# Optimization experiments

Measured on AMD Instinct MI355X. Metric: run time of the kernel, lower is better.

## Reference

```python
import jax, jax.numpy as jnp
import numpy as np

B, N, NEV, E, D, L = 4, 20000, 100000, 400000, 64, 3

def setup_inputs() -> dict:
    key = jax.random.key(0)
    ks = jax.random.split(key, 12)
    x = jax.random.normal(ks[0], (B, N, 3), dtype=jnp.float32)
    # channel 0 is the susceptible boolean mask (0/1)
    mask0 = (jax.random.uniform(ks[1], (B, N)) < 0.3).astype(jnp.float32)
    x = x.at[..., 0].set(mask0)
    dag_edge_index = jax.random.randint(ks[2], (2, E), 0, NEV, dtype=jnp.int64)
    event_to_node = jax.random.randint(ks[3], (NEV,), 0, N, dtype=jnp.int64)
    event_src_node = jax.random.randint(ks[4], (NEV,), 0, N, dtype=jnp.int64)
    s = 1.0 / np.sqrt(D)
    Wp = jax.random.normal(ks[5], (6, D), dtype=jnp.float32) * (1.0 / np.sqrt(6))
    bp = jnp.zeros((D,), dtype=jnp.float32)
    Ws = jax.random.normal(ks[6], (L, D, D), dtype=jnp.float32) * s
    Wa = jax.random.normal(ks[7], (L, D, D), dtype=jnp.float32) * s
    ba = jnp.zeros((L, D), dtype=jnp.float32)
    Wo = jax.random.normal(ks[8], (D,), dtype=jnp.float32) * s
    bo = jnp.zeros((), dtype=jnp.float32)
    return {"x": x, "Wp": Wp, "bp": bp, "Ws": Ws, "Wa": Wa, "ba": ba,
            "Wo": Wo, "bo": bo, "dag_edge_index": dag_edge_index,
            "event_to_node": event_to_node, "event_src_node": event_src_node}

def reference(x, Wp, bp, Ws, Wa, ba, Wo, bo, dag_edge_index, event_to_node, event_src_node):
    n_events = event_src_node.shape[0]
    # event features: [B, n_events, 6] -> project -> ReLU
    ev_feat = jnp.concatenate([x[:, event_src_node, :], x[:, event_to_node, :]], axis=-1)
    h = jax.nn.relu(ev_feat @ Wp + bp)  # [B, n_events, D]
    # reversed DAG edges: src = dag[1], dst = dag[0]
    src_e, dst_e = dag_edge_index[1], dag_edge_index[0]
    deg = jnp.zeros((n_events,), h.dtype).at[dst_e].add(1.0)
    deg = jnp.maximum(deg, 1.0)[None, :, None]
    for l in range(Ws.shape[0]):
        agg = jnp.zeros_like(h).at[:, dst_e].add(h[:, src_e])  # scatter-add mean agg
        h = jax.nn.relu(h @ Ws[l] + (agg / deg) @ Wa[l] + ba[l])
    # aggregate events back to nodes (mean)
    node_emb = jnp.zeros((x.shape[0], x.shape[1], h.shape[-1]), h.dtype).at[:, event_to_node].add(h)
    count = jnp.zeros((x.shape[1],), h.dtype).at[event_to_node].add(1.0)
    node_emb = node_emb / jnp.maximum(count, 1.0)[None, :, None]
    scores = node_emb @ Wo + bo  # [B, N]
    susceptible = x[..., 0] > 0
    scores = jnp.where(susceptible, -jnp.inf, scores)
    return jax.nn.log_softmax(scores, axis=-1)
```

## Files before the change

### kernel.cpp

```cpp
#include <hip/hip_runtime.h>
#include <hip/hip_bf16.h>
#include <math.h>

constexpr int B   = 4;
constexpr int N   = 20000;
constexpr int NEV = 100000;
constexpr int E   = 400000;
constexpr int D   = 64;
constexpr int L   = 3;
constexpr int CAP = 32;
constexpr int CHUNK = 625;

typedef short  short8 __attribute__((ext_vector_type(8)));
typedef float  f32x4  __attribute__((ext_vector_type(4)));
typedef float  f32x2  __attribute__((ext_vector_type(2)));


__device__ inline unsigned short f2bu(float f) {
  union { __hip_bfloat16 b; unsigned short s; } u;
  u.b = __float2bfloat16(f);
  return u.s;
}
__device__ inline unsigned packbf(float lo, float hi) {
  return ((unsigned)f2bu(hi) << 16) | (unsigned)f2bu(lo);
}
__device__ inline void cvt16(float* a, uint4 v) {
  unsigned vv[4] = {v.x, v.y, v.z, v.w};
#pragma unroll
  for (int i = 0; i < 4; ++i) {
    f32x2 lo = __builtin_amdgcn_cvt_pk_f32_fp8((int)vv[i], false);
    f32x2 hi = __builtin_amdgcn_cvt_pk_f32_fp8((int)vv[i], true);
    a[4 * i + 0] = lo[0]; a[4 * i + 1] = lo[1];
    a[4 * i + 2] = hi[0]; a[4 * i + 3] = hi[1];
  }
}
__device__ inline void add16(float* a, uint4 v) {
  unsigned vv[4] = {v.x, v.y, v.z, v.w};
#pragma unroll
  for (int i = 0; i < 4; ++i) {
    f32x2 lo = __builtin_amdgcn_cvt_pk_f32_fp8((int)vv[i], false);
    f32x2 hi = __builtin_amdgcn_cvt_pk_f32_fp8((int)vv[i], true);
    a[4 * i + 0] += lo[0]; a[4 * i + 1] += lo[1];
    a[4 * i + 2] += hi[0]; a[4 * i + 3] += hi[1];
  }
}
__device__ inline short8 pack8(const float* f) {
  union { unsigned u[4]; short8 s; } r;
#pragma unroll
  for (int i = 0; i < 4; ++i) r.u[i] = packbf(f[2 * i], f[2 * i + 1]);
  return r.s;
}


__global__ void k_zero(float4* __restrict__ p, int n4) {
  int i = blockIdx.x * blockDim.x + threadIdx.x;
  if (i < n4) p[i] = make_float4(0.f, 0.f, 0.f, 0.f);
}

__global__ void k_prep(const int* __restrict__ dag,
                       int* __restrict__ cnt,
                       int* __restrict__ csrc,
                       const int* __restrict__ e2n,
                       int* __restrict__ ncount,
                       const float* __restrict__ Ws,
                       const float* __restrict__ Wa,
                       unsigned short* __restrict__ Wt) {
  int bid = blockIdx.x;
  if (bid < 1563) {
    int i = bid * 256 + threadIdx.x;
    if (i < E) {
      int dst = dag[i];
      int src = dag[E + i];
      int pos = atomicAdd(&cnt[dst], 1);
      if (pos < CAP) csrc[dst * CAP + pos] = src;
    }
  } else if (bid < 1954) {
    int i = (bid - 1563) * 256 + threadIdx.x;
    if (i < NEV) atomicAdd(&ncount[e2n[i]], 1);
  } else {
    int i = (bid - 1954) * 256 + threadIdx.x;
    int l  = i >> 13;
    int r  = i & 8191;
    int n  = r >> 7;
    int s2 = r & 127;
    int hf = s2 >> 6, s = s2 & 63;
    int b  = ((s >> 3) & 3) * 16 + (s >> 5) * 8 + (s & 7);
    int c  = (b & 3) * 16 + (b >> 2);
    float v = hf ? Wa[l * 4096 + c * 64 + n]
                 : Ws[l * 4096 + c * 64 + n];
    Wt[l * 8192 + n * 128 + s2] = f2bu(v);
  }
}

__global__ __launch_bounds__(256) void k_proj(const float* __restrict__ x,
                                              const float* __restrict__ Wp,
                                              const float* __restrict__ bp,
                                              const int* __restrict__ esrc,
                                              const int* __restrict__ e2n,
                                              unsigned* __restrict__ h,
                                              float* __restrict__ nscore) {
  int gid = blockIdx.x * blockDim.x + threadIdx.x;
  if (gid < B * N) nscore[gid] = 0.f;
  const int lane = threadIdx.x & 63;
  const int e    = gid >> 6;
  int sn = esrc[e], tn = e2n[e];
  float xval = 0.f;
  if (lane < 24) {
    int bl = lane / 6, rem = lane % 6;
    int node = (rem < 3) ? sn : tn;
    xval = x[(size_t)(bl * N + node) * 3 + (rem < 3 ? rem : rem - 3)];
  }
  const int b = lane >> 4, p = lane & 15;
  float xv[6];
#pragma unroll
  for (int k = 0; k < 6; ++k) xv[k] = __shfl(xval, b * 6 + k, 64);
  float a[4];
#pragma unroll
  for (int t = 0; t < 4; ++t) {
    int d = p + 16 * t;
    float acc = bp[d];
#pragma unroll
    for (int k = 0; k < 6; ++k) acc += xv[k] * Wp[k * 64 + d];
    a[t] = fmaxf(acc, 0.f);
  }
  int w = __builtin_amdgcn_cvt_pk_fp8_f32(a[0], a[1], 0, false);
  w     = __builtin_amdgcn_cvt_pk_fp8_f32(a[2], a[3], w, true);
  h[e * 64 + lane] = (unsigned)w;
}

template <bool LAST>
__global__ __launch_bounds__(256, 4) void k_layer(
    const unsigned short* __restrict__ Wt,
    const float* __restrict__ ba,
    const float* __restrict__ Wo,
    const int* __restrict__ e2n,
    const int* __restrict__ cnt,
    const int* __restrict__ csrc,
    const unsigned char* __restrict__ h_in,
    unsigned char* __restrict__ h_out,
    float* __restrict__ nscore) {
  const int tid  = threadIdx.x;
  const int wv   = tid >> 6, lane = tid & 63;
  const int e0   = blockIdx.x * 16;
  const int r0   = e0 * 4;
  const int m    = lane & 15, q = lane >> 4;
  const int el   = m >> 2;
  const int bb   = m & 3;
  const int e_loc = wv * 4 + el;

  int vidx = csrc[(size_t)(e0 + wv * 4 + q) * CAP + m];

  uint4 vd = *(const uint4*)(h_in + (size_t)(r0 + wv * 16 + m) * 64 + q * 16);

  int c    = cnt[e0 + e_loc];
  int cc   = min(c, CAP);
  int cc16 = min(cc, 16);
  float a[16];
#pragma unroll
  for (int i = 0; i < 16; ++i) a[i] = 0.f;
  const unsigned char* gb = h_in + bb * 64 + q * 16;
  for (int p = 0; p < cc16; p += 4) {
    uint4 v[4];
#pragma unroll
    for (int t = 0; t < 4; ++t) {
      v[t] = make_uint4(0u, 0u, 0u, 0u);
      int j = p + t;
      int s = __shfl(vidx, (el << 4) | (j & 15), 64);
      if (j < cc16) v[t] = *(const uint4*)(gb + (size_t)s * 256);
    }
#pragma unroll
    for (int t = 0; t < 4; ++t) add16(a, v[t]);
  }
  for (int j = 16; j < cc; ++j) {
    int s = csrc[(size_t)(e0 + e_loc) * CAP + j];
    add16(a, *(const uint4*)(gb + (size_t)s * 256));
  }
  {
    float inv = 1.f / fmaxf((float)c, 1.f);
#pragma unroll
    for (int i = 0; i < 16; ++i) a[i] *= inv;
  }
  short8 ag0 = pack8(a), ag1 = pack8(a + 8);

  short8 ad0, ad1;
  {
    float fd[16];
    cvt16(fd, vd);
    ad0 = pack8(fd); ad1 = pack8(fd + 8);
  }

  f32x4 acc[4];
#pragma unroll
  for (int t = 0; t < 4; ++t) {
    float bv = ba[t * 16 + m];
    acc[t] = (f32x4){bv, bv, bv, bv};
  }
  const unsigned short* wb = Wt + m * 128 + q * 8;
#pragma unroll
  for (int t = 0; t < 4; ++t) {
    acc[t] = __builtin_amdgcn_mfma_f32_16x16x32_bf16(
        ad0, *(const short8*)(wb + t * 2048 + 0),  acc[t], 0, 0, 0);
    acc[t] = __builtin_amdgcn_mfma_f32_16x16x32_bf16(
        ad1, *(const short8*)(wb + t * 2048 + 32), acc[t], 0, 0, 0);
    acc[t] = __builtin_amdgcn_mfma_f32_16x16x32_bf16(
        ag0, *(const short8*)(wb + t * 2048 + 64), acc[t], 0, 0, 0);
    acc[t] = __builtin_amdgcn_mfma_f32_16x16x32_bf16(
        ag1, *(const short8*)(wb + t * 2048 + 96), acc[t], 0, 0, 0);
  }

  if constexpr (!LAST) {
#pragma unroll
    for (int r = 0; r < 4; ++r) {
      int w = __builtin_amdgcn_cvt_pk_fp8_f32(fmaxf(acc[0][r], 0.f),
                                              fmaxf(acc[1][r], 0.f), 0, false);
      w     = __builtin_amdgcn_cvt_pk_fp8_f32(fmaxf(acc[2][r], 0.f),
                                              fmaxf(acc[3][r], 0.f), w, true);
      int grow = r0 + wv * 16 + q * 4 + r;
      ((unsigned*)h_out)[grow * 16 + m] = (unsigned)w;
    }
  } else {
    float w0 = Wo[m], w1 = Wo[16 + m], w2 = Wo[32 + m], w3 = Wo[48 + m];
#pragma unroll
    for (int r = 0; r < 4; ++r) {
      float v = fmaxf(acc[0][r], 0.f) * w0 + fmaxf(acc[1][r], 0.f) * w1
              + fmaxf(acc[2][r], 0.f) * w2 + fmaxf(acc[3][r], 0.f) * w3;
      v += __shfl_xor(v, 1, 64);
      v += __shfl_xor(v, 2, 64);
      v += __shfl_xor(v, 4, 64);
      v += __shfl_xor(v, 8, 64);
      if (m == 0) {
        int grow = r0 + wv * 16 + q * 4 + r;
        int e = grow >> 2, b = grow & 3;
        atomicAdd(&nscore[b * N + e2n[e]], v);
      }
    }
  }
}

__device__ inline float ls_score(const float* nscore, const int* ncount,
                                 const float* x, float bov, int b, int n) {
  return (x[(size_t)(b * N + n) * 3] > 0.f)
             ? -INFINITY
             : nscore[b * N + n] / fmaxf((float)ncount[n], 1.f) + bov;
}

__global__ __launch_bounds__(256) void k_ls1(const float* __restrict__ nscore,
                                             const int* __restrict__ ncount,
                                             const float* __restrict__ x,
                                             const float* __restrict__ bo,
                                             float* __restrict__ pmax,
                                             float* __restrict__ psum,
                                             float* __restrict__ sc) {
  const int b = blockIdx.x >> 5, ch = blockIdx.x & 31;
  const int n0 = ch * CHUNK;
  const int tid = threadIdx.x;
  const float bov = bo[0];
  float s0 = -INFINITY, s1 = -INFINITY, s2 = -INFINITY;
  if (tid < CHUNK) {
    s0 = ls_score(nscore, ncount, x, bov, b, n0 + tid);
    sc[b * N + n0 + tid] = s0;
  }
  if (tid + 256 < CHUNK) {
    s1 = ls_score(nscore, ncount, x, bov, b, n0 + tid + 256);
    sc[b * N + n0 + tid + 256] = s1;
  }
  if (tid + 512 < CHUNK) {
    s2 = ls_score(nscore, ncount, x, bov, b, n0 + tid + 512);
    sc[b * N + n0 + tid + 512] = s2;
  }
  float m = fmaxf(fmaxf(s0, s1), s2);
  __shared__ float red[4];
#pragma unroll
  for (int o = 32; o; o >>= 1) m = fmaxf(m, __shfl_xor(m, o, 64));
  if ((tid & 63) == 0) red[tid >> 6] = m;
  __syncthreads();
  float pm = fmaxf(fmaxf(red[0], red[1]), fmaxf(red[2], red[3]));
  float pm2 = (pm == -INFINITY) ? 0.f : pm;
  float e = expf(s0 - pm2) + expf(s1 - pm2) + expf(s2 - pm2);
#pragma unroll
  for (int o = 32; o; o >>= 1) e += __shfl_xor(e, o, 64);
  __syncthreads();
  if ((tid & 63) == 0) red[tid >> 6] = e;
  __syncthreads();
  if (tid == 0) {
    pmax[blockIdx.x] = pm;
    psum[blockIdx.x] = red[0] + red[1] + red[2] + red[3];
  }
}

__global__ __launch_bounds__(256) void k_ls3(const float* __restrict__ pmax,
                                             const float* __restrict__ psum,
                                             const float* __restrict__ sc,
                                             float* __restrict__ out) {
  const int b = blockIdx.x >> 5, ch = blockIdx.x & 31;
  const int n0 = ch * CHUNK;
  const int tid = threadIdx.x;
  __shared__ float sgm, slse;
  if (tid < 64) {
    float pm = (tid < 32) ? pmax[b * 32 + tid] : -INFINITY;
    float ps = (tid < 32) ? psum[b * 32 + tid] : 0.f;
    float gm = pm;
#pragma unroll
    for (int o = 32; o; o >>= 1) gm = fmaxf(gm, __shfl_xor(gm, o, 64));
    float gm2 = (gm == -INFINITY) ? 0.f : gm;
    float c = (pm == -INFINITY) ? 0.f : ps * expf(pm - gm2);
#pragma unroll
    for (int o = 32; o; o >>= 1) c += __shfl_xor(c, o, 64);
    if (tid == 0) { sgm = gm; slse = logf(c); }
  }
  __syncthreads();
  const float gm = sgm, lse = slse;
  for (int i = tid; i < CHUNK; i += 256) {
    int n = n0 + i;
    out[b * N + n] = fmaxf(sc[b * N + n] - gm - lse, -3.0e38f);
  }
}

extern "C" void kernel_launch(void* const* d_in, const int* in_sizes, int n_in,
                              void* d_out, int out_size, void* d_ws, size_t ws_size,
                              hipStream_t stream) {
  const float* x   = (const float*)d_in[0];
  const float* Wp  = (const float*)d_in[1];
  const float* bp  = (const float*)d_in[2];
  const float* Ws  = (const float*)d_in[3];
  const float* Wa  = (const float*)d_in[4];
  const float* ba  = (const float*)d_in[5];
  const float* Wo  = (const float*)d_in[6];
  const float* bo  = (const float*)d_in[7];
  const int*   dag = (const int*)d_in[8];
  const int*   e2n = (const int*)d_in[9];
  const int*   esr = (const int*)d_in[10];

  int*   ws     = (int*)d_ws;
  int*   cnt    = ws;
  int*   ncount = ws + 100000;
  float* nscore = (float*)(ws + 120000);
  float* pmax   = (float*)(ws + 200000);
  float* psum   = (float*)(ws + 200128);
  int*   csrc   = ws + 200704;
  unsigned short* Wt = (unsigned short*)(ws + 3400704);
  unsigned char* h0 = (unsigned char*)(ws + 3406912);
  unsigned char* h1 = h0 + (size_t)B * NEV * D;
  float* sc     = (float*)(h1 + (size_t)B * NEV * D);
  float* out    = (float*)d_out;

  k_zero<<<(30000 + 255) / 256, 256, 0, stream>>>((float4*)ws, 30000);
  k_prep<<<2050, 256, 0, stream>>>(dag, cnt, csrc, e2n, ncount, Ws, Wa, Wt);
  k_proj<<<(B * NEV * 16) / 256, 256, 0, stream>>>(x, Wp, bp, esr, e2n,
                                                   (unsigned*)h0, nscore);

  k_layer<false><<<NEV / 16, 256, 0, stream>>>(Wt,         ba,       Wo, e2n,
                                               cnt, csrc, h0, h1, nscore);
  k_layer<false><<<NEV / 16, 256, 0, stream>>>(Wt + 8192,  ba + D,   Wo, e2n,
                                               cnt, csrc, h1, h0, nscore);
  k_layer<true><<<NEV / 16, 256, 0, stream>>>(Wt + 16384,  ba + 2*D, Wo, e2n,
                                              cnt, csrc, h0, h1, nscore);

  k_ls1<<<B * 32, 256, 0, stream>>>(nscore, ncount, x, bo, pmax, psum, sc);
  k_ls3<<<B * 32, 256, 0, stream>>>(pmax, psum, sc, out);
}
```

Baseline: 354.5 us.

## Process two event tiles per wave with sentinel-padded neighbor lists for gather ILP

Each layer block now handles 32 events instead of 16, with each wave computing two independent 16-row tiles (A and B). This interleaves their gathers and MFMAs for more memory-level parallelism and reuses the loaded weight fragments across both tiles. The CSR neighbor table is pre-filled with a sentinel index pointing at an extra zeroed row in each h buffer. This lets the first four neighbors be loaded unconditionally with vector int4 index loads instead of cross-lane shuffles and bounds checks. In exchange it adds a fill kernel, more registers per thread and half as many blocks, which may lower occupancy.

```diff
diff --git a/kernel.cpp b/kernel.cpp
--- a/kernel.cpp
+++ b/kernel.cpp
@@ -10,6 +10,7 @@
 constexpr int L   = 3;
 constexpr int CAP = 32;
 constexpr int CHUNK = 625;
+constexpr size_t HBYTES = (size_t)B * NEV * D + 256;
 
 typedef short  short8 __attribute__((ext_vector_type(8)));
 typedef float  f32x4  __attribute__((ext_vector_type(4)));
@@ -50,11 +51,29 @@
   for (int i = 0; i < 4; ++i) r.u[i] = packbf(f[2 * i], f[2 * i + 1]);
   return r.s;
 }
+__device__ __forceinline__ void round4(const unsigned char* gb,
+                                       const int* cr, int p, float* a) {
+  int4 idx = *(const int4*)(cr + p);
+  uint4 v0 = *(const uint4*)(gb + (size_t)idx.x * 256);
+  uint4 v1 = *(const uint4*)(gb + (size_t)idx.y * 256);
+  uint4 v2 = *(const uint4*)(gb + (size_t)idx.z * 256);
+  uint4 v3 = *(const uint4*)(gb + (size_t)idx.w * 256);
+  add16(a, v0); add16(a, v1); add16(a, v2); add16(a, v3);
+}
 
 
 __global__ void k_zero(float4* __restrict__ p, int n4) {
   int i = blockIdx.x * blockDim.x + threadIdx.x;
   if (i < n4) p[i] = make_float4(0.f, 0.f, 0.f, 0.f);
+}
+
+__global__ void k_fill(int4* __restrict__ csrc4,
+                       uint4* __restrict__ h0z, uint4* __restrict__ h1z) {
+  int i = blockIdx.x * blockDim.x + threadIdx.x;
+  if (i < NEV * CAP / 4) csrc4[i] = make_int4(NEV, NEV, NEV, NEV);
+  int z = i - NEV * CAP / 4;
+  if (z >= 0 && z < 16) h0z[z] = make_uint4(0u, 0u, 0u, 0u);
+  if (z >= 16 && z < 32) h1z[z - 16] = make_uint4(0u, 0u, 0u, 0u);
 }
 
 __global__ void k_prep(const int* __restrict__ dag,
@@ -141,97 +160,119 @@
     float* __restrict__ nscore) {
   const int tid  = threadIdx.x;
   const int wv   = tid >> 6, lane = tid & 63;
-  const int e0   = blockIdx.x * 16;
+  const int e0   = blockIdx.x * 32;
   const int r0   = e0 * 4;
   const int m    = lane & 15, q = lane >> 4;
   const int el   = m >> 2;
   const int bb   = m & 3;
-  const int e_loc = wv * 4 + el;
-
-  int vidx = csrc[(size_t)(e0 + wv * 4 + q) * CAP + m];
-
-  uint4 vd = *(const uint4*)(h_in + (size_t)(r0 + wv * 16 + m) * 64 + q * 16);
-
-  int c    = cnt[e0 + e_loc];
-  int cc   = min(c, CAP);
-  int cc16 = min(cc, 16);
-  float a[16];
-#pragma unroll
-  for (int i = 0; i < 16; ++i) a[i] = 0.f;
+  const int eA   = e0 + wv * 4 + el;
+  const int eB   = e0 + 16 + wv * 4 + el;
+
+  const int* crA = csrc + (size_t)eA * CAP;
+  const int* crB = csrc + (size_t)eB * CAP;
+  int4 iA = *(const int4*)crA;
+  int4 iB = *(const int4*)crB;
+  uint4 vdA = *(const uint4*)(h_in + (size_t)(r0 + wv * 16 + m) * 64 + q * 16);
+  uint4 vdB = *(const uint4*)(h_in + (size_t)(r0 + 64 + wv * 16 + m) * 64 + q * 16);
+  int cA = cnt[eA];
+  int cB = cnt[eB];
+
   const unsigned char* gb = h_in + bb * 64 + q * 16;
-  for (int p = 0; p < cc16; p += 4) {
-    uint4 v[4];
-#pragma unroll
-    for (int t = 0; t < 4; ++t) {
-      v[t] = make_uint4(0u, 0u, 0u, 0u);
-      int j = p + t;
-      int s = __shfl(vidx, (el << 4) | (j & 15), 64);
-      if (j < cc16) v[t] = *(const uint4*)(gb + (size_t)s * 256);
-    }
-#pragma unroll
-    for (int t = 0; t < 4; ++t) add16(a, v[t]);
-  }
-  for (int j = 16; j < cc; ++j) {
-    int s = csrc[(size_t)(e0 + e_loc) * CAP + j];
-    add16(a, *(const uint4*)(gb + (size_t)s * 256));
-  }
+  float aA[16], aB[16];
+#pragma unroll
+  for (int i = 0; i < 16; ++i) { aA[i] = 0.f; aB[i] = 0.f; }
   {
-    float inv = 1.f / fmaxf((float)c, 1.f);
-#pragma unroll
-    for (int i = 0; i < 16; ++i) a[i] *= inv;
-  }
-  short8 ag0 = pack8(a), ag1 = pack8(a + 8);
-
-  short8 ad0, ad1;
+    uint4 vA0 = *(const uint4*)(gb + (size_t)iA.x * 256);
+    uint4 vA1 = *(const uint4*)(gb + (size_t)iA.y * 256);
+    uint4 vA2 = *(const uint4*)(gb + (size_t)iA.z * 256);
+    uint4 vA3 = *(const uint4*)(gb + (size_t)iA.w * 256);
+    uint4 vB0 = *(const uint4*)(gb + (size_t)iB.x * 256);
+    uint4 vB1 = *(const uint4*)(gb + (size_t)iB.y * 256);
+    uint4 vB2 = *(const uint4*)(gb + (size_t)iB.z * 256);
+    uint4 vB3 = *(const uint4*)(gb + (size_t)iB.w * 256);
+    add16(aA, vA0); add16(aA, vA1); add16(aA, vA2); add16(aA, vA3);
+    add16(aB, vB0); add16(aB, vB1); add16(aB, vB2); add16(aB, vB3);
+  }
+  int ccA = min(cA, CAP), ccA16 = min(ccA, 16);
+  int ccB = min(cB, CAP), ccB16 = min(ccB, 16);
+  for (int p = 4; p < ccA16; p += 4) round4(gb, crA, p, aA);
+  for (int p = 4; p < ccB16; p += 4) round4(gb, crB, p, aB);
+  for (int j = 16; j < ccA; ++j)
+    add16(aA, *(const uint4*)(gb + (size_t)crA[j] * 256));
+  for (int j = 16; j < ccB; ++j)
+    add16(aB, *(const uint4*)(gb + (size_t)crB[j] * 256));
   {
-    float fd[16];
-    cvt16(fd, vd);
-    ad0 = pack8(fd); ad1 = pack8(fd + 8);
-  }
-
-  f32x4 acc[4];
+    float invA = 1.f / fmaxf((float)cA, 1.f);
+    float invB = 1.f / fmaxf((float)cB, 1.f);
+#pragma unroll
+    for (int i = 0; i < 16; ++i) { aA[i] *= invA; aB[i] *= invB; }
+  }
+  short8 agA0 = pack8(aA), agA1 = pack8(aA + 8);
+  short8 agB0 = pack8(aB), agB1 = pack8(aB + 8);
+
+  short8 adA0, adA1, adB0, adB1;
+  {
+    float f[16];
+    cvt16(f, vdA); adA0 = pack8(f); adA1 = pack8(f + 8);
+    cvt16(f, vdB); adB0 = pack8(f); adB1 = pack8(f + 8);
+  }
+
+  f32x4 accA[4], accB[4];
 #pragma unroll
   for (int t = 0; t < 4; ++t) {
     float bv = ba[t * 16 + m];
-    acc[t] = (f32x4){bv, bv, bv, bv};
+    accA[t] = (f32x4){bv, bv, bv, bv};
+    accB[t] = accA[t];
   }
   const unsigned short* wb = Wt + m * 128 + q * 8;
 #pragma unroll
   for (int t = 0; t < 4; ++t) {
-    acc[t] = __builtin_amdgcn_mfma_f32_16x16x32_bf16(
-        ad0, *(const short8*)(wb + t * 2048 + 0),  acc[t], 0, 0, 0);
-    acc[t] = __builtin_amdgcn_mfma_f32_16x16x32_bf16(
-        ad1, *(const short8*)(wb + t * 2048 + 32), acc[t], 0, 0, 0);
-    acc[t] = __builtin_amdgcn_mfma_f32_16x16x32_bf16(
-        ag0, *(const short8*)(wb + t * 2048 + 64), acc[t], 0, 0, 0);
-    acc[t] = __builtin_amdgcn_mfma_f32_16x16x32_bf16(
-        ag1, *(const short8*)(wb + t * 2048 + 96), acc[t], 0, 0, 0);
+    short8 b0 = *(const short8*)(wb + t * 2048 + 0);
+    short8 b1 = *(const short8*)(wb + t * 2048 + 32);
+    short8 b2 = *(const short8*)(wb + t * 2048 + 64);
+    short8 b3 = *(const short8*)(wb + t * 2048 + 96);
+    accA[t] = __builtin_amdgcn_mfma_f32_16x16x32_bf16(adA0, b0, accA[t], 0, 0, 0);
+    accA[t] = __builtin_amdgcn_mfma_f32_16x16x32_bf16(adA1, b1, accA[t], 0, 0, 0);
+    accA[t] = __builtin_amdgcn_mfma_f32_16x16x32_bf16(agA0, b2, accA[t], 0, 0, 0);
+    accA[t] = __builtin_amdgcn_mfma_f32_16x16x32_bf16(agA1, b3, accA[t], 0, 0, 0);
+    accB[t] = __builtin_amdgcn_mfma_f32_16x16x32_bf16(adB0, b0, accB[t], 0, 0, 0);
+    accB[t] = __builtin_amdgcn_mfma_f32_16x16x32_bf16(adB1, b1, accB[t], 0, 0, 0);
+    accB[t] = __builtin_amdgcn_mfma_f32_16x16x32_bf16(agB0, b2, accB[t], 0, 0, 0);
+    accB[t] = __builtin_amdgcn_mfma_f32_16x16x32_bf16(agB1, b3, accB[t], 0, 0, 0);
   }
 
   if constexpr (!LAST) {
 #pragma unroll
-    for (int r = 0; r < 4; ++r) {
-      int w = __builtin_amdgcn_cvt_pk_fp8_f32(fmaxf(acc[0][r], 0.f),
-                                              fmaxf(acc[1][r], 0.f), 0, false);
-      w     = __builtin_amdgcn_cvt_pk_fp8_f32(fmaxf(acc[2][r], 0.f),
-                                              fmaxf(acc[3][r], 0.f), w, true);
-      int grow = r0 + wv * 16 + q * 4 + r;
-      ((unsigned*)h_out)[grow * 16 + m] = (unsigned)w;
+    for (int g = 0; g < 2; ++g) {
+      const f32x4* ac = g ? accB : accA;
+#pragma unroll
+      for (int r = 0; r < 4; ++r) {
+        int w = __builtin_amdgcn_cvt_pk_fp8_f32(fmaxf(ac[0][r], 0.f),
+                                                fmaxf(ac[1][r], 0.f), 0, false);
+        w     = __builtin_amdgcn_cvt_pk_fp8_f32(fmaxf(ac[2][r], 0.f),
+                                                fmaxf(ac[3][r], 0.f), w, true);
+        int grow = r0 + g * 64 + wv * 16 + q * 4 + r;
+        ((unsigned*)h_out)[grow * 16 + m] = (unsigned)w;
+      }
     }
   } else {
     float w0 = Wo[m], w1 = Wo[16 + m], w2 = Wo[32 + m], w3 = Wo[48 + m];
 #pragma unroll
-    for (int r = 0; r < 4; ++r) {
-      float v = fmaxf(acc[0][r], 0.f) * w0 + fmaxf(acc[1][r], 0.f) * w1
-              + fmaxf(acc[2][r], 0.f) * w2 + fmaxf(acc[3][r], 0.f) * w3;
-      v += __shfl_xor(v, 1, 64);
-      v += __shfl_xor(v, 2, 64);
-      v += __shfl_xor(v, 4, 64);
-      v += __shfl_xor(v, 8, 64);
-      if (m == 0) {
-        int grow = r0 + wv * 16 + q * 4 + r;
-        int e = grow >> 2, b = grow & 3;
-        atomicAdd(&nscore[b * N + e2n[e]], v);
+    for (int g = 0; g < 2; ++g) {
+      const f32x4* ac = g ? accB : accA;
+#pragma unroll
+      for (int r = 0; r < 4; ++r) {
+        float v = fmaxf(ac[0][r], 0.f) * w0 + fmaxf(ac[1][r], 0.f) * w1
+                + fmaxf(ac[2][r], 0.f) * w2 + fmaxf(ac[3][r], 0.f) * w3;
+        v += __shfl_xor(v, 1, 64);
+        v += __shfl_xor(v, 2, 64);
+        v += __shfl_xor(v, 4, 64);
+        v += __shfl_xor(v, 8, 64);
+        if (m == 0) {
+          int grow = r0 + g * 64 + wv * 16 + q * 4 + r;
+          int e = grow >> 2, b = grow & 3;
+          atomicAdd(&nscore[b * N + e2n[e]], v);
+        }
       }
     }
   }
@@ -340,20 +381,22 @@
   int*   csrc   = ws + 200704;
   unsigned short* Wt = (unsigned short*)(ws + 3400704);
   unsigned char* h0 = (unsigned char*)(ws + 3406912);
-  unsigned char* h1 = h0 + (size_t)B * NEV * D;
-  float* sc     = (float*)(h1 + (size_t)B * NEV * D);
+  unsigned char* h1 = h0 + HBYTES;
+  float* sc     = (float*)(h1 + HBYTES);
   float* out    = (float*)d_out;
 
   k_zero<<<(30000 + 255) / 256, 256, 0, stream>>>((float4*)ws, 30000);
+  k_fill<<<(NEV * CAP / 4 + 32 + 255) / 256, 256, 0, stream>>>(
+      (int4*)csrc, (uint4*)(h0 + (size_t)NEV * 256), (uint4*)(h1 + (size_t)NEV * 256));
   k_prep<<<2050, 256, 0, stream>>>(dag, cnt, csrc, e2n, ncount, Ws, Wa, Wt);
   k_proj<<<(B * NEV * 16) / 256, 256, 0, stream>>>(x, Wp, bp, esr, e2n,
                                                    (unsigned*)h0, nscore);
 
-  k_layer<false><<<NEV / 16, 256, 0, stream>>>(Wt,         ba,       Wo, e2n,
+  k_layer<false><<<NEV / 32, 256, 0, stream>>>(Wt,         ba,       Wo, e2n,
                                                cnt, csrc, h0, h1, nscore);
-  k_layer<false><<<NEV / 16, 256, 0, stream>>>(Wt + 8192,  ba + D,   Wo, e2n,
+  k_layer<false><<<NEV / 32, 256, 0, stream>>>(Wt + 8192,  ba + D,   Wo, e2n,
                                                cnt, csrc, h1, h0, nscore);
-  k_layer<true><<<NEV / 16, 256, 0, stream>>>(Wt + 16384,  ba + 2*D, Wo, e2n,
+  k_layer<true><<<NEV / 32, 256, 0, stream>>>(Wt + 16384,  ba + 2*D, Wo, e2n,
                                               cnt, csrc, h0, h1, nscore);
 
   k_ls1<<<B * 32, 256, 0, stream>>>(nscore, ncount, x, bo, pmax, psum, sc);
```

After: 295.1 us. -16.8%, faster.

## Stage first eight neighbor rows into LDS via global_load_lds with padded sentinel rows

Applied to the files above, without the earlier changes.

Splits the neighbor list into a fixed 8-slot low part and a 24-slot overflow part. Empty slots are filled with a sentinel index pointing at an extra zeroed row appended to each h buffer, so the first eight neighbors can be gathered unconditionally with direct global-to-LDS loads. This removes the per-neighbor branching and shuffles from the common path and issues all gathers up front. Accumulation moves to packed f32x2 operations. The cost is 32 KB of LDS per block, which may limit occupancy, a full vmcnt wait before accumulation, extra fill work, and a serial fallback loop for events with more than eight neighbors.

```diff
diff --git a/kernel.cpp b/kernel.cpp
--- a/kernel.cpp
+++ b/kernel.cpp
@@ -10,6 +10,7 @@
 constexpr int L   = 3;
 constexpr int CAP = 32;
 constexpr int CHUNK = 625;
+constexpr size_t HBYTES = (size_t)B * NEV * D + 256;
 
 typedef short  short8 __attribute__((ext_vector_type(8)));
 typedef float  f32x4  __attribute__((ext_vector_type(4)));
@@ -24,31 +25,34 @@
 __device__ inline unsigned packbf(float lo, float hi) {
   return ((unsigned)f2bu(hi) << 16) | (unsigned)f2bu(lo);
 }
-__device__ inline void cvt16(float* a, uint4 v) {
+__device__ __forceinline__ void add16p(f32x2* a2, uint4 v) {
   unsigned vv[4] = {v.x, v.y, v.z, v.w};
 #pragma unroll
   for (int i = 0; i < 4; ++i) {
     f32x2 lo = __builtin_amdgcn_cvt_pk_f32_fp8((int)vv[i], false);
     f32x2 hi = __builtin_amdgcn_cvt_pk_f32_fp8((int)vv[i], true);
-    a[4 * i + 0] = lo[0]; a[4 * i + 1] = lo[1];
-    a[4 * i + 2] = hi[0]; a[4 * i + 3] = hi[1];
-  }
-}
-__device__ inline void add16(float* a, uint4 v) {
+    a2[2 * i]     += lo;
+    a2[2 * i + 1] += hi;
+  }
+}
+__device__ __forceinline__ void cvt16p(f32x2* a2, uint4 v) {
   unsigned vv[4] = {v.x, v.y, v.z, v.w};
 #pragma unroll
   for (int i = 0; i < 4; ++i) {
-    f32x2 lo = __builtin_amdgcn_cvt_pk_f32_fp8((int)vv[i], false);
-    f32x2 hi = __builtin_amdgcn_cvt_pk_f32_fp8((int)vv[i], true);
-    a[4 * i + 0] += lo[0]; a[4 * i + 1] += lo[1];
-    a[4 * i + 2] += hi[0]; a[4 * i + 3] += hi[1];
-  }
-}
-__device__ inline short8 pack8(const float* f) {
+    a2[2 * i]     = __builtin_amdgcn_cvt_pk_f32_fp8((int)vv[i], false);
+    a2[2 * i + 1] = __builtin_amdgcn_cvt_pk_f32_fp8((int)vv[i], true);
+  }
+}
+__device__ __forceinline__ short8 pack8p(const f32x2* f) {
   union { unsigned u[4]; short8 s; } r;
 #pragma unroll
-  for (int i = 0; i < 4; ++i) r.u[i] = packbf(f[2 * i], f[2 * i + 1]);
+  for (int i = 0; i < 4; ++i) r.u[i] = packbf(f[i][0], f[i][1]);
   return r.s;
+}
+typedef __attribute__((address_space(3))) unsigned int lds_u32;
+typedef __attribute__((address_space(1))) const unsigned int gbl_u32;
+__device__ __forceinline__ void stage_row16(const unsigned char* g, unsigned char* l) {
+  __builtin_amdgcn_global_load_lds((gbl_u32*)g, (lds_u32*)l, 16, 0, 0);
 }
 
 
@@ -57,9 +61,19 @@
   if (i < n4) p[i] = make_float4(0.f, 0.f, 0.f, 0.f);
 }
 
+__global__ void k_fill(int4* __restrict__ lo4,
+                       uint4* __restrict__ h0z, uint4* __restrict__ h1z) {
+  int i = blockIdx.x * blockDim.x + threadIdx.x;
+  if (i < NEV * 8 / 4) lo4[i] = make_int4(NEV, NEV, NEV, NEV);
+  int z = i - NEV * 8 / 4;
+  if (z >= 0 && z < 16) h0z[z] = make_uint4(0u, 0u, 0u, 0u);
+  if (z >= 16 && z < 32) h1z[z - 16] = make_uint4(0u, 0u, 0u, 0u);
+}
+
 __global__ void k_prep(const int* __restrict__ dag,
                        int* __restrict__ cnt,
-                       int* __restrict__ csrc,
+                       int* __restrict__ csrc_lo,
+                       int* __restrict__ csrc_hi,
                        const int* __restrict__ e2n,
                        int* __restrict__ ncount,
                        const float* __restrict__ Ws,
@@ -72,7 +86,8 @@
       int dst = dag[i];
       int src = dag[E + i];
       int pos = atomicAdd(&cnt[dst], 1);
-      if (pos < CAP) csrc[dst * CAP + pos] = src;
+      if (pos < 8)        csrc_lo[dst * 8 + pos] = src;
+      else if (pos < CAP) csrc_hi[dst * 24 + (pos - 8)] = src;
     }
   } else if (bid < 1954) {
     int i = (bid - 1563) * 256 + threadIdx.x;
@@ -135,59 +150,63 @@
     const float* __restrict__ Wo,
     const int* __restrict__ e2n,
     const int* __restrict__ cnt,
-    const int* __restrict__ csrc,
+    const int* __restrict__ csrc_lo,
+    const int* __restrict__ csrc_hi,
     const unsigned char* __restrict__ h_in,
     unsigned char* __restrict__ h_out,
     float* __restrict__ nscore) {
+  __shared__ unsigned char sbuf[4][8192];
   const int tid  = threadIdx.x;
   const int wv   = tid >> 6, lane = tid & 63;
-  const int e0   = blockIdx.x * 16;
-  const int r0   = e0 * 4;
   const int m    = lane & 15, q = lane >> 4;
   const int el   = m >> 2;
   const int bb   = m & 3;
-  const int e_loc = wv * 4 + el;
-
-  int vidx = csrc[(size_t)(e0 + wv * 4 + q) * CAP + m];
-
-  uint4 vd = *(const uint4*)(h_in + (size_t)(r0 + wv * 16 + m) * 64 + q * 16);
-
-  int c    = cnt[e0 + e_loc];
-  int cc   = min(c, CAP);
-  int cc16 = min(cc, 16);
-  float a[16];
-#pragma unroll
-  for (int i = 0; i < 16; ++i) a[i] = 0.f;
-  const unsigned char* gb = h_in + bb * 64 + q * 16;
-  for (int p = 0; p < cc16; p += 4) {
-    uint4 v[4];
-#pragma unroll
-    for (int t = 0; t < 4; ++t) {
-      v[t] = make_uint4(0u, 0u, 0u, 0u);
-      int j = p + t;
-      int s = __shfl(vidx, (el << 4) | (j & 15), 64);
-      if (j < cc16) v[t] = *(const uint4*)(gb + (size_t)s * 256);
-    }
-#pragma unroll
-    for (int t = 0; t < 4; ++t) add16(a, v[t]);
-  }
-  for (int j = 16; j < cc; ++j) {
-    int s = csrc[(size_t)(e0 + e_loc) * CAP + j];
-    add16(a, *(const uint4*)(gb + (size_t)s * 256));
+  const int ew   = blockIdx.x * 16 + wv * 4;
+  const int e    = ew + el;
+
+  int vidx = csrc_lo[ew * 8 + (lane & 31)];
+  int cl   = cnt[ew + (lane & 3)];
+  uint4 vd = *(const uint4*)(h_in + (size_t)(ew * 4 + m) * 64 + q * 16);
+
+  unsigned char* lbase = sbuf[wv];
+#pragma unroll
+  for (int k = 0; k < 8; ++k) {
+    int s = __shfl(vidx, (k >> 1) * 8 + (k & 1) * 4 + q, 64);
+    const unsigned char* g = h_in + (size_t)s * 256 + (lane & 15) * 16;
+    stage_row16(g, lbase + k * 1024);
+  }
+
+  short8 ad0, ad1;
+  {
+    f32x2 f[8];
+    cvt16p(f, vd);
+    ad0 = pack8p(f); ad1 = pack8p(f + 4);
+  }
+  int c  = __shfl(cl, el, 64);
+  int cc = min(c, CAP);
+
+  asm volatile("s_waitcnt vmcnt(0)" ::: "memory");
+  __builtin_amdgcn_sched_barrier(0);
+  f32x2 a[8];
+#pragma unroll
+  for (int i = 0; i < 8; ++i) a[i] = (f32x2){0.f, 0.f};
+  const unsigned char* rb = lbase + el * 2048 + bb * 64 + q * 16;
+#pragma unroll
+  for (int j = 0; j < 8; ++j)
+    add16p(a, *(const uint4*)(rb + (j >> 2) * 1024 + (j & 3) * 256));
+
+  if (cc > 8) {
+    const unsigned char* gb = h_in + bb * 64 + q * 16;
+    const int* ch = csrc_hi + (size_t)e * 24;
+    for (int j = 8; j < cc; ++j)
+      add16p(a, *(const uint4*)(gb + (size_t)ch[j - 8] * 256));
   }
   {
     float inv = 1.f / fmaxf((float)c, 1.f);
 #pragma unroll
-    for (int i = 0; i < 16; ++i) a[i] *= inv;
-  }
-  short8 ag0 = pack8(a), ag1 = pack8(a + 8);
-
-  short8 ad0, ad1;
-  {
-    float fd[16];
-    cvt16(fd, vd);
-    ad0 = pack8(fd); ad1 = pack8(fd + 8);
-  }
+    for (int i = 0; i < 8; ++i) a[i] = a[i] * inv;
+  }
+  short8 ag0 = pack8p(a), ag1 = pack8p(a + 4);
 
   f32x4 acc[4];
 #pragma unroll
@@ -215,7 +234,7 @@
                                               fmaxf(acc[1][r], 0.f), 0, false);
       w     = __builtin_amdgcn_cvt_pk_fp8_f32(fmaxf(acc[2][r], 0.f),
                                               fmaxf(acc[3][r], 0.f), w, true);
-      int grow = r0 + wv * 16 + q * 4 + r;
+      int grow = ew * 4 + q * 4 + r;
       ((unsigned*)h_out)[grow * 16 + m] = (unsigned)w;
     }
   } else {
@@ -229,9 +248,9 @@
       v += __shfl_xor(v, 4, 64);
       v += __shfl_xor(v, 8, 64);
       if (m == 0) {
-        int grow = r0 + wv * 16 + q * 4 + r;
-        int e = grow >> 2, b = grow & 3;
-        atomicAdd(&nscore[b * N + e2n[e]], v);
+        int grow = ew * 4 + q * 4 + r;
+        int ee = grow >> 2, b = grow & 3;
+        atomicAdd(&nscore[b * N + e2n[ee]], v);
       }
     }
   }
@@ -337,24 +356,28 @@
   float* nscore = (float*)(ws + 120000);
   float* pmax   = (float*)(ws + 200000);
   float* psum   = (float*)(ws + 200128);
-  int*   csrc   = ws + 200704;
+  int*   csrc_lo = ws + 200704;
+  int*   csrc_hi = ws + 1000704;
   unsigned short* Wt = (unsigned short*)(ws + 3400704);
   unsigned char* h0 = (unsigned char*)(ws + 3406912);
-  unsigned char* h1 = h0 + (size_t)B * NEV * D;
-  float* sc     = (float*)(h1 + (size_t)B * NEV * D);
+  unsigned char* h1 = h0 + HBYTES;
+  float* sc     = (float*)(h1 + HBYTES);
   float* out    = (float*)d_out;
 
   k_zero<<<(30000 + 255) / 256, 256, 0, stream>>>((float4*)ws, 30000);
-  k_prep<<<2050, 256, 0, stream>>>(dag, cnt, csrc, e2n, ncount, Ws, Wa, Wt);
+  k_fill<<<(NEV * 2 + 32 + 255) / 256, 256, 0, stream>>>(
+      (int4*)csrc_lo, (uint4*)(h0 + (size_t)NEV * 256), (uint4*)(h1 + (size_t)NEV * 256));
+  k_prep<<<2050, 256, 0, stream>>>(dag, cnt, csrc_lo, csrc_hi, e2n, ncount,
+                                   Ws, Wa, Wt);
   k_proj<<<(B * NEV * 16) / 256, 256, 0, stream>>>(x, Wp, bp, esr, e2n,
                                                    (unsigned*)h0, nscore);
 
   k_layer<false><<<NEV / 16, 256, 0, stream>>>(Wt,         ba,       Wo, e2n,
-                                               cnt, csrc, h0, h1, nscore);
+                                               cnt, csrc_lo, csrc_hi, h0, h1, nscore);
   k_layer<false><<<NEV / 16, 256, 0, stream>>>(Wt + 8192,  ba + D,   Wo, e2n,
-                                               cnt, csrc, h1, h0, nscore);
+                                               cnt, csrc_lo, csrc_hi, h1, h0, nscore);
   k_layer<true><<<NEV / 16, 256, 0, stream>>>(Wt + 16384,  ba + 2*D, Wo, e2n,
-                                              cnt, csrc, h0, h1, nscore);
+                                              cnt, csrc_lo, csrc_hi, h0, h1, nscore);
 
   k_ls1<<<B * 32, 256, 0, stream>>>(nscore, ncount, x, bo, pmax, psum, sc);
   k_ls3<<<B * 32, 256, 0, stream>>>(pmax, psum, sc, out);
```

After: 332.9 us. -6.1%, faster.
